# Performance work log

Measured on AMD Instinct MI355X. Metric: run time of the kernel, lower is better.

The kernel has to match this reference:

```python
import jax, jax.numpy as jnp
import numpy as np

DIM = 256
NUM_HEADS = 8


def setup_inputs() -> dict:
    key = jax.random.key(0)
    ks = jax.random.split(key, 8)
    B, H, W = 2, 64, 64
    s = 0.02
    return {
        "query": jax.random.normal(ks[0], (B, H, W, DIM), jnp.float32),
        "sim": jax.random.normal(ks[1], (B, H, W, DIM), jnp.float32),
        "Wq": jax.random.normal(ks[2], (DIM, DIM), jnp.float32) * s,
        "bq": jnp.zeros((DIM,), jnp.float32),
        "Wkv": jax.random.normal(ks[3], (DIM, 2 * DIM), jnp.float32) * s,
        "bkv": jnp.zeros((2 * DIM,), jnp.float32),
        "Wp": jax.random.normal(ks[4], (DIM, DIM), jnp.float32) * s,
        "bp": jnp.zeros((DIM,), jnp.float32),
    }


def reference(query, sim, Wq, bq, Wkv, bkv, Wp, bp):
    B, H, W, dim = query.shape
    nh = NUM_HEADS
    dh = dim // nh
    scale = dh ** (-0.5)
    S = H * W

    # projections
    q = (query.reshape(B, S, dim) @ Wq + bq).reshape(B, S, nh, dh)
    kv = (sim.reshape(B, S, dim) @ Wkv + bkv).reshape(B, S, 2, nh, dh)
    k = kv[:, :, 0]  # [B,S,nh,dh]
    v = kv[:, :, 1]

    # attention: scores [B,nh,S,S]
    attn = jnp.einsum('bqhd,bkhd->bhqk', q * scale, k)
    attn = jax.nn.softmax(attn, axis=-1)
    x = jnp.einsum('bhqk,bkhd->bqhd', attn, v)  # [B,S,nh,dh]
    x = x.reshape(B, H, W, dim)
    return x @ Wp + bp
```

## Files before the change

### kernel.cpp

```cpp
#include <hip/hip_runtime.h>
#include <hip/hip_bf16.h>
#include <math.h>


#define SCALE 0.17677669529663687f
#define LOG2E 1.4426950408889634f

typedef __attribute__((ext_vector_type(8))) short short8;
typedef __attribute__((ext_vector_type(4))) float f32x4;

static __device__ __forceinline__ unsigned short f2bf(float x) {
    union { float f; unsigned int u; } v; v.f = x;
    unsigned int r = v.u + 0x7fff + ((v.u >> 16) & 1);
    return (unsigned short)(r >> 16);
}
static __device__ __forceinline__ float bf2f(unsigned short h) {
    union { unsigned int u; float f; } v; v.u = ((unsigned int)h) << 16;
    return v.f;
}
static __device__ __forceinline__ float fexp2(float x) {
#if __has_builtin(__builtin_amdgcn_exp2f)
    return __builtin_amdgcn_exp2f(x);
#else
    float r; asm("v_exp_f32 %0, %1" : "=v"(r) : "v"(x)); return r;
#endif
}
static __device__ __forceinline__ unsigned int pk_bf16(float a, float b) {
    unsigned int r;
    asm("v_cvt_pk_bf16_f32 %0, %1, %2" : "=v"(r) : "v"(a), "v"(b));
    return r;
}

__global__ __launch_bounds__(256) void prep_w(
    const float* __restrict__ Wq, const float* __restrict__ Wkv,
    const float* __restrict__ Wp,
    unsigned short* __restrict__ whi, unsigned short* __restrict__ wlo)
{
    const int n = blockIdx.x & 255, mat = blockIdx.x >> 8, k = threadIdx.x;
    const float* src; int ldw, colx; float sc = 1.f;
    if (mat == 0)      { src = Wq;  ldw = 256; colx = n;       sc = SCALE * LOG2E; }
    else if (mat == 1) { src = Wkv; ldw = 512; colx = n;       }
    else if (mat == 2) { src = Wkv; ldw = 512; colx = n + 256; }
    else               { src = Wp;  ldw = 256; colx = n;       }
    float v = src[(long long)k * ldw + colx] * sc;
    unsigned short h = f2bf(v);
    unsigned short l = f2bf(v - bf2f(h));
    const int o = blockIdx.x * 256 + k;
    whi[o] = h; wlo[o] = l;
}

__global__ __launch_bounds__(256) void gemm_qkv(
    const float* __restrict__ query, const float* __restrict__ sim,
    const unsigned short* __restrict__ whi, const unsigned short* __restrict__ wlo,
    const float* __restrict__ bq, const float* __restrict__ bkv,
    unsigned short* __restrict__ qbuf, unsigned short* __restrict__ kbuf,
    unsigned short* __restrict__ vTb)
{
    __shared__ unsigned short XsH[64 * 40], XsL[64 * 40];
    __shared__ unsigned short WsH[64 * 40], WsL[64 * 40];

    const int t = threadIdx.x, wave = t >> 6, lane = t & 63;
    const int col = lane & 15, quad = lane >> 4;
    const int by = blockIdx.y;
    const int kind = by >> 2;
    const int n0 = (by & 3) * 64;
    const int m0 = blockIdx.x * 64;
    const float* __restrict__ X = (kind == 0) ? query : sim;
    const int wrow0 = kind * 256 + n0;
    const int srow = t >> 2, spart = (t & 3) * 8;

    const f32x4 zero = {0.f, 0.f, 0.f, 0.f};
    f32x4 acc[4] = {zero, zero, zero, zero};

    for (int kt = 0; kt < 8; ++kt) {
        const int k0 = kt * 32;
        const float* xp = &X[(long long)(m0 + srow) * 256 + k0 + spart];
        float4 xa = *(const float4*)xp;
        float4 xb = *(const float4*)(xp + 4);
        float xv[8] = {xa.x, xa.y, xa.z, xa.w, xb.x, xb.y, xb.z, xb.w};
        union { unsigned short s[8]; uint4 u; } ph, pl;
#pragma unroll
        for (int j = 0; j < 8; ++j) {
            unsigned short h = f2bf(xv[j]);
            ph.s[j] = h;
            pl.s[j] = f2bf(xv[j] - bf2f(h));
        }
        uint4 wh = *(const uint4*)&whi[(long long)(wrow0 + srow) * 256 + k0 + spart];
        uint4 wl = *(const uint4*)&wlo[(long long)(wrow0 + srow) * 256 + k0 + spart];
        __syncthreads();
        *(uint4*)&XsH[srow * 40 + spart] = ph.u;
        *(uint4*)&XsL[srow * 40 + spart] = pl.u;
        *(uint4*)&WsH[srow * 40 + spart] = wh;
        *(uint4*)&WsL[srow * 40 + spart] = wl;
        __syncthreads();

        const unsigned short* Ah = (kind == 2) ? WsH : XsH;
        const unsigned short* Al = (kind == 2) ? WsL : XsL;
        const unsigned short* Bh = (kind == 2) ? XsH : WsH;
        const unsigned short* Bl = (kind == 2) ? XsL : WsL;

        short8 a_h = *(const short8*)(Ah + (wave * 16 + col) * 40 + quad * 8);
        short8 a_l = *(const short8*)(Al + (wave * 16 + col) * 40 + quad * 8);
#pragma unroll
        for (int nt = 0; nt < 4; ++nt) {
            short8 b_h = *(const short8*)(Bh + (nt * 16 + col) * 40 + quad * 8);
            short8 b_l = *(const short8*)(Bl + (nt * 16 + col) * 40 + quad * 8);
            acc[nt] = __builtin_amdgcn_mfma_f32_16x16x32_bf16(a_h, b_h, acc[nt], 0, 0, 0);
            acc[nt] = __builtin_amdgcn_mfma_f32_16x16x32_bf16(a_l, b_h, acc[nt], 0, 0, 0);
            acc[nt] = __builtin_amdgcn_mfma_f32_16x16x32_bf16(a_h, b_l, acc[nt], 0, 0, 0);
        }
    }

    if (kind == 0) {
#pragma unroll
        for (int nt = 0; nt < 4; ++nt) {
            int n = n0 + nt * 16 + col;
            int h = n >> 5, d = n & 31;
            float bias = bq[n] * (SCALE * LOG2E);
#pragma unroll
            for (int r = 0; r < 4; ++r) {
                int mg = m0 + wave * 16 + quad * 4 + r;
                int b = mg >> 12, sidx = mg & 4095;
                qbuf[((long long)(b * 8 + h) * 4096 + sidx) * 32 + d] = f2bf(acc[nt][r] + bias);
            }
        }
    } else if (kind == 1) {
#pragma unroll
        for (int nt = 0; nt < 4; ++nt) {
            int n = n0 + nt * 16 + col;
            int h = n >> 5, d = n & 31;
            float bias = bkv[n];
#pragma unroll
            for (int r = 0; r < 4; ++r) {
                int mg = m0 + wave * 16 + quad * 4 + r;
                int b = mg >> 12, sidx = mg & 4095;
                kbuf[((long long)(b * 8 + h) * 4096 + sidx) * 32 + d] = f2bf(acc[nt][r] + bias);
            }
        }
    } else {
#pragma unroll
        for (int nt = 0; nt < 4; ++nt) {
            int s = m0 + nt * 16 + col;
            int b = s >> 12, sidx = s & 4095;
#pragma unroll
            for (int r = 0; r < 4; ++r) {
                int dcol = n0 + wave * 16 + quad * 4 + r;
                int h = dcol >> 5, dd = dcol & 31;
                float bias = bkv[256 + dcol];
                vTb[((long long)((b * 8 + h) * 32 + dd)) * 4096 + sidx] = f2bf(acc[nt][r] + bias);
            }
        }
    }
}

__global__ __launch_bounds__(256) void flash_mfma(
    const unsigned short* __restrict__ qbuf,
    const unsigned short* __restrict__ kbuf,
    const unsigned short* __restrict__ vT,
    float* __restrict__ xbuf)
{
    __shared__ unsigned short Ks[128 * 40];
    __shared__ unsigned short Vt[32 * 136];
    __shared__ unsigned short Pb[4][640];

    const int t = threadIdx.x;
    const int wave = t >> 6, lane = t & 63;
    const int col = lane & 15, quad = lane >> 4;
    const int bh = blockIdx.x >> 5;
    const int q0 = (blockIdx.x & 31) * 128 + wave * 32;
    const long long kvbase = (long long)bh * 4096 * 32;
    unsigned short* pbw = Pb[wave];

    const short8 qf0 = *(const short8*)(qbuf + kvbase + (long long)(q0 + col) * 32 + quad * 8);
    const short8 qf1 = *(const short8*)(qbuf + kvbase + (long long)(q0 + 16 + col) * 32 + quad * 8);

    const f32x4 zero = {0.f, 0.f, 0.f, 0.f};
    f32x4 o00 = zero, o01 = zero, o10 = zero, o11 = zero;
    float l0 = 0.f, l1 = 0.f;

    const int krow = t >> 2, kpart = (t & 3) * 8;
    const int vrow = t >> 4, vpart = (t & 15) * 8;

    for (int kt = 0; kt < 32; ++kt) {
        uint4 kg0 = *(const uint4*)(kbuf + kvbase + (long long)(kt * 128 + krow) * 32 + kpart);
        uint4 kg1 = *(const uint4*)(kbuf + kvbase + (long long)(kt * 128 + krow + 64) * 32 + kpart);
        uint4 vg0 = *(const uint4*)(vT + ((long long)(bh * 32 + vrow)) * 4096 + kt * 128 + vpart);
        uint4 vg1 = *(const uint4*)(vT + ((long long)(bh * 32 + vrow + 16)) * 4096 + kt * 128 + vpart);
        __syncthreads();
        *(uint4*)(Ks + krow * 40 + kpart) = kg0;
        *(uint4*)(Ks + (krow + 64) * 40 + kpart) = kg1;
        *(uint4*)(Vt + vrow * 136 + vpart) = vg0;
        *(uint4*)(Vt + (vrow + 16) * 136 + vpart) = vg1;
        __syncthreads();

#pragma unroll
        for (int sb = 0; sb < 4; ++sb) {
            const int kb = sb * 32;
            short8 a0 = *(const short8*)(Ks + (kb + col) * 40 + quad * 8);
            short8 a1 = *(const short8*)(Ks + (kb + 16 + col) * 40 + quad * 8);
            short8 v0 = *(const short8*)(Vt + col * 136 + kb + quad * 8);
            short8 v1 = *(const short8*)(Vt + (16 + col) * 136 + kb + quad * 8);
            {
                f32x4 c0 = __builtin_amdgcn_mfma_f32_16x16x32_bf16(a0, qf0, zero, 0, 0, 0);
                f32x4 c1 = __builtin_amdgcn_mfma_f32_16x16x32_bf16(a1, qf0, zero, 0, 0, 0);
                float p0 = fexp2(c0[0]), p1 = fexp2(c0[1]), p2 = fexp2(c0[2]), p3 = fexp2(c0[3]);
                float p4 = fexp2(c1[0]), p5 = fexp2(c1[1]), p6 = fexp2(c1[2]), p7 = fexp2(c1[3]);
                l0 += ((p0 + p1) + (p2 + p3)) + ((p4 + p5) + (p6 + p7));
                uint2 w0 = make_uint2(pk_bf16(p0, p1), pk_bf16(p2, p3));
                uint2 w1 = make_uint2(pk_bf16(p4, p5), pk_bf16(p6, p7));
                *(uint2*)(pbw + col * 40 + quad * 4) = w0;
                *(uint2*)(pbw + col * 40 + 16 + quad * 4) = w1;
                short8 pf = *(const short8*)(pbw + col * 40 + quad * 8);
                o00 = __builtin_amdgcn_mfma_f32_16x16x32_bf16(v0, pf, o00, 0, 0, 0);
                o01 = __builtin_amdgcn_mfma_f32_16x16x32_bf16(v1, pf, o01, 0, 0, 0);
            }
            {
                f32x4 c0 = __builtin_amdgcn_mfma_f32_16x16x32_bf16(a0, qf1, zero, 0, 0, 0);
                f32x4 c1 = __builtin_amdgcn_mfma_f32_16x16x32_bf16(a1, qf1, zero, 0, 0, 0);
                float p0 = fexp2(c0[0]), p1 = fexp2(c0[1]), p2 = fexp2(c0[2]), p3 = fexp2(c0[3]);
                float p4 = fexp2(c1[0]), p5 = fexp2(c1[1]), p6 = fexp2(c1[2]), p7 = fexp2(c1[3]);
                l1 += ((p0 + p1) + (p2 + p3)) + ((p4 + p5) + (p6 + p7));
                uint2 w0 = make_uint2(pk_bf16(p0, p1), pk_bf16(p2, p3));
                uint2 w1 = make_uint2(pk_bf16(p4, p5), pk_bf16(p6, p7));
                *(uint2*)(pbw + col * 40 + quad * 4) = w0;
                *(uint2*)(pbw + col * 40 + 16 + quad * 4) = w1;
                short8 pf = *(const short8*)(pbw + col * 40 + quad * 8);
                o10 = __builtin_amdgcn_mfma_f32_16x16x32_bf16(v0, pf, o10, 0, 0, 0);
                o11 = __builtin_amdgcn_mfma_f32_16x16x32_bf16(v1, pf, o11, 0, 0, 0);
            }
        }
    }

    l0 += __shfl_xor(l0, 16, 64); l0 += __shfl_xor(l0, 32, 64);
    l1 += __shfl_xor(l1, 16, 64); l1 += __shfl_xor(l1, 32, 64);
    const float i0 = 1.f / l0, i1 = 1.f / l1;

    const int b = bh >> 3, hh = bh & 7;
    float* xp0 = xbuf + ((long long)(b * 4096 + q0 + col)) * 256 + hh * 32;
    *(float4*)(xp0 + quad * 4)      = make_float4(o00[0] * i0, o00[1] * i0, o00[2] * i0, o00[3] * i0);
    *(float4*)(xp0 + 16 + quad * 4) = make_float4(o01[0] * i0, o01[1] * i0, o01[2] * i0, o01[3] * i0);
    float* xp1 = xbuf + ((long long)(b * 4096 + q0 + 16 + col)) * 256 + hh * 32;
    *(float4*)(xp1 + quad * 4)      = make_float4(o10[0] * i1, o10[1] * i1, o10[2] * i1, o10[3] * i1);
    *(float4*)(xp1 + 16 + quad * 4) = make_float4(o11[0] * i1, o11[1] * i1, o11[2] * i1, o11[3] * i1);
}

__global__ __launch_bounds__(256) void gemm_outp(
    const float* __restrict__ xbuf,
    const unsigned short* __restrict__ whi, const unsigned short* __restrict__ wlo,
    const float* __restrict__ bp, float* __restrict__ out)
{
    __shared__ unsigned short XsH[64 * 40], XsL[64 * 40];
    __shared__ unsigned short WsH[64 * 40], WsL[64 * 40];

    const int t = threadIdx.x, wave = t >> 6, lane = t & 63;
    const int col = lane & 15, quad = lane >> 4;
    const int n0 = blockIdx.y * 64;
    const int m0 = blockIdx.x * 64;
    const int wrow0 = 768 + n0;
    const int srow = t >> 2, spart = (t & 3) * 8;

    const f32x4 zero = {0.f, 0.f, 0.f, 0.f};
    f32x4 acc[4] = {zero, zero, zero, zero};

    for (int kt = 0; kt < 8; ++kt) {
        const int k0 = kt * 32;
        const float* xp = &xbuf[(long long)(m0 + srow) * 256 + k0 + spart];
        float4 xa = *(const float4*)xp;
        float4 xb = *(const float4*)(xp + 4);
        float xv[8] = {xa.x, xa.y, xa.z, xa.w, xb.x, xb.y, xb.z, xb.w};
        union { unsigned short s[8]; uint4 u; } ph, pl;
#pragma unroll
        for (int j = 0; j < 8; ++j) {
            unsigned short h = f2bf(xv[j]);
            ph.s[j] = h;
            pl.s[j] = f2bf(xv[j] - bf2f(h));
        }
        uint4 wh = *(const uint4*)&whi[(long long)(wrow0 + srow) * 256 + k0 + spart];
        uint4 wl = *(const uint4*)&wlo[(long long)(wrow0 + srow) * 256 + k0 + spart];
        __syncthreads();
        *(uint4*)&XsH[srow * 40 + spart] = ph.u;
        *(uint4*)&XsL[srow * 40 + spart] = pl.u;
        *(uint4*)&WsH[srow * 40 + spart] = wh;
        *(uint4*)&WsL[srow * 40 + spart] = wl;
        __syncthreads();

        short8 a_h = *(const short8*)(XsH + (wave * 16 + col) * 40 + quad * 8);
        short8 a_l = *(const short8*)(XsL + (wave * 16 + col) * 40 + quad * 8);
#pragma unroll
        for (int nt = 0; nt < 4; ++nt) {
            short8 b_h = *(const short8*)(WsH + (nt * 16 + col) * 40 + quad * 8);
            short8 b_l = *(const short8*)(WsL + (nt * 16 + col) * 40 + quad * 8);
            acc[nt] = __builtin_amdgcn_mfma_f32_16x16x32_bf16(a_h, b_h, acc[nt], 0, 0, 0);
            acc[nt] = __builtin_amdgcn_mfma_f32_16x16x32_bf16(a_l, b_h, acc[nt], 0, 0, 0);
            acc[nt] = __builtin_amdgcn_mfma_f32_16x16x32_bf16(a_h, b_l, acc[nt], 0, 0, 0);
        }
    }

#pragma unroll
    for (int nt = 0; nt < 4; ++nt) {
        int n = n0 + nt * 16 + col;
        float bias = bp[n];
#pragma unroll
        for (int r = 0; r < 4; ++r) {
            int mg = m0 + wave * 16 + quad * 4 + r;
            out[(long long)mg * 256 + n] = acc[nt][r] + bias;
        }
    }
}

extern "C" void kernel_launch(void* const* d_in, const int* in_sizes, int n_in,
                              void* d_out, int out_size, void* d_ws, size_t ws_size,
                              hipStream_t stream) {
    const float* query = (const float*)d_in[0];
    const float* sim   = (const float*)d_in[1];
    const float* Wq    = (const float*)d_in[2];
    const float* bq    = (const float*)d_in[3];
    const float* Wkv   = (const float*)d_in[4];
    const float* bkv   = (const float*)d_in[5];
    const float* Wp    = (const float*)d_in[6];
    const float* bp    = (const float*)d_in[7];
    float* out = (float*)d_out;

    unsigned short* wsb = (unsigned short*)d_ws;
    unsigned short* qbuf = wsb;
    unsigned short* kbuf = wsb + 2097152;
    unsigned short* vT   = wsb + 4194304;
    float* xbuf = (float*)(wsb + 6291456);
    unsigned short* whi  = wsb + 10485760;
    unsigned short* wlo  = whi + 262144;

    prep_w   <<<dim3(1024),    256, 0, stream>>>(Wq, Wkv, Wp, whi, wlo);
    gemm_qkv <<<dim3(128, 12), 256, 0, stream>>>(query, sim, whi, wlo, bq, bkv,
                                                 qbuf, kbuf, vT);
    flash_mfma<<<dim3(512),    256, 0, stream>>>(qbuf, kbuf, vT, xbuf);
    gemm_outp<<<dim3(128, 4),  256, 0, stream>>>(xbuf, whi, wlo, bp, out);
}
```

Before: 176.1 us.

## Split flash attention over KV halves, enlarge per-wave query tile, pre-split inputs

The flash kernel now gives each wave 64 queries instead of 32, so every K/V tile staged in LDS is reused across more queries. The KV range is split into two halves across blocks, with unnormalized partial outputs and row sums written to workspace and combined and normalized in the output GEMM. Row sums are computed with an MFMA against a ones vector instead of scalar adds, and LDS strides change from 40 to 42 to reduce bank conflicts. Query and sim inputs are converted to bf16 hi/lo once in a prep kernel, so the QKV GEMM no longer repeats that conversion for each of its output-column blocks. The cost is more intermediate memory traffic (two fp32 partial buffers, bf16 copies of the inputs) and higher register pressure in the flash kernel.

```diff
diff --git a/kernel.cpp b/kernel.cpp
--- a/kernel.cpp
+++ b/kernel.cpp
@@ -31,33 +31,53 @@
     return r;
 }
 
-__global__ __launch_bounds__(256) void prep_w(
+__global__ __launch_bounds__(256) void prep(
+    const float* __restrict__ query, const float* __restrict__ sim,
     const float* __restrict__ Wq, const float* __restrict__ Wkv,
     const float* __restrict__ Wp,
+    unsigned short* __restrict__ xhi, unsigned short* __restrict__ xlo,
     unsigned short* __restrict__ whi, unsigned short* __restrict__ wlo)
 {
-    const int n = blockIdx.x & 255, mat = blockIdx.x >> 8, k = threadIdx.x;
-    const float* src; int ldw, colx; float sc = 1.f;
-    if (mat == 0)      { src = Wq;  ldw = 256; colx = n;       sc = SCALE * LOG2E; }
-    else if (mat == 1) { src = Wkv; ldw = 512; colx = n;       }
-    else if (mat == 2) { src = Wkv; ldw = 512; colx = n + 256; }
-    else               { src = Wp;  ldw = 256; colx = n;       }
-    float v = src[(long long)k * ldw + colx] * sc;
-    unsigned short h = f2bf(v);
-    unsigned short l = f2bf(v - bf2f(h));
-    const int o = blockIdx.x * 256 + k;
-    whi[o] = h; wlo[o] = l;
+    const int blk = blockIdx.x, t = threadIdx.x;
+    if (blk < 4096) {
+        const int e = blk * 1024 + t * 4;
+        const float* src = (e < 2097152) ? (query + e) : (sim + (e - 2097152));
+        float4 v = *(const float4*)src;
+        float xv[4] = {v.x, v.y, v.z, v.w};
+        union { unsigned short s[4]; uint2 u; } ph, pl;
+#pragma unroll
+        for (int j = 0; j < 4; ++j) {
+            unsigned short h = f2bf(xv[j]);
+            ph.s[j] = h;
+            pl.s[j] = f2bf(xv[j] - bf2f(h));
+        }
+        *(uint2*)&xhi[e] = ph.u;
+        *(uint2*)&xlo[e] = pl.u;
+    } else {
+        const int bb = blk - 4096;
+        const int n = bb & 255, mat = bb >> 8, k = t;
+        const float* src; int ldw, colx; float sc = 1.f;
+        if (mat == 0)      { src = Wq;  ldw = 256; colx = n;       sc = SCALE * LOG2E; }
+        else if (mat == 1) { src = Wkv; ldw = 512; colx = n;       }
+        else if (mat == 2) { src = Wkv; ldw = 512; colx = n + 256; }
+        else               { src = Wp;  ldw = 256; colx = n;       }
+        float v = src[(long long)k * ldw + colx] * sc;
+        unsigned short h = f2bf(v);
+        unsigned short l = f2bf(v - bf2f(h));
+        const int o = bb * 256 + k;
+        whi[o] = h; wlo[o] = l;
+    }
 }
 
 __global__ __launch_bounds__(256) void gemm_qkv(
-    const float* __restrict__ query, const float* __restrict__ sim,
+    const unsigned short* __restrict__ xhi, const unsigned short* __restrict__ xlo,
     const unsigned short* __restrict__ whi, const unsigned short* __restrict__ wlo,
     const float* __restrict__ bq, const float* __restrict__ bkv,
     unsigned short* __restrict__ qbuf, unsigned short* __restrict__ kbuf,
     unsigned short* __restrict__ vTb)
 {
-    __shared__ unsigned short XsH[64 * 40], XsL[64 * 40];
-    __shared__ unsigned short WsH[64 * 40], WsL[64 * 40];
+    __shared__ unsigned short XsH[64 * 42], XsL[64 * 42];
+    __shared__ unsigned short WsH[64 * 42], WsL[64 * 42];
 
     const int t = threadIdx.x, wave = t >> 6, lane = t & 63;
     const int col = lane & 15, quad = lane >> 4;
@@ -65,7 +85,7 @@
     const int kind = by >> 2;
     const int n0 = (by & 3) * 64;
     const int m0 = blockIdx.x * 64;
-    const float* __restrict__ X = (kind == 0) ? query : sim;
+    const int xrow0 = ((kind == 0) ? 0 : 8192) + m0;
     const int wrow0 = kind * 256 + n0;
     const int srow = t >> 2, spart = (t & 3) * 8;
 
@@ -74,24 +94,15 @@
 
     for (int kt = 0; kt < 8; ++kt) {
         const int k0 = kt * 32;
-        const float* xp = &X[(long long)(m0 + srow) * 256 + k0 + spart];
-        float4 xa = *(const float4*)xp;
-        float4 xb = *(const float4*)(xp + 4);
-        float xv[8] = {xa.x, xa.y, xa.z, xa.w, xb.x, xb.y, xb.z, xb.w};
-        union { unsigned short s[8]; uint4 u; } ph, pl;
-#pragma unroll
-        for (int j = 0; j < 8; ++j) {
-            unsigned short h = f2bf(xv[j]);
-            ph.s[j] = h;
-            pl.s[j] = f2bf(xv[j] - bf2f(h));
-        }
+        uint4 xh = *(const uint4*)&xhi[(long long)(xrow0 + srow) * 256 + k0 + spart];
+        uint4 xl = *(const uint4*)&xlo[(long long)(xrow0 + srow) * 256 + k0 + spart];
         uint4 wh = *(const uint4*)&whi[(long long)(wrow0 + srow) * 256 + k0 + spart];
         uint4 wl = *(const uint4*)&wlo[(long long)(wrow0 + srow) * 256 + k0 + spart];
         __syncthreads();
-        *(uint4*)&XsH[srow * 40 + spart] = ph.u;
-        *(uint4*)&XsL[srow * 40 + spart] = pl.u;
-        *(uint4*)&WsH[srow * 40 + spart] = wh;
-        *(uint4*)&WsL[srow * 40 + spart] = wl;
+        *(uint4*)&XsH[srow * 42 + spart] = xh;
+        *(uint4*)&XsL[srow * 42 + spart] = xl;
+        *(uint4*)&WsH[srow * 42 + spart] = wh;
+        *(uint4*)&WsL[srow * 42 + spart] = wl;
         __syncthreads();
 
         const unsigned short* Ah = (kind == 2) ? WsH : XsH;
@@ -99,12 +110,12 @@
         const unsigned short* Bh = (kind == 2) ? XsH : WsH;
         const unsigned short* Bl = (kind == 2) ? XsL : WsL;
 
-        short8 a_h = *(const short8*)(Ah + (wave * 16 + col) * 40 + quad * 8);
-        short8 a_l = *(const short8*)(Al + (wave * 16 + col) * 40 + quad * 8);
-#pragma unroll
-        for (int nt = 0; nt < 4; ++nt) {
-            short8 b_h = *(const short8*)(Bh + (nt * 16 + col) * 40 + quad * 8);
-            short8 b_l = *(const short8*)(Bl + (nt * 16 + col) * 40 + quad * 8);
+        short8 a_h = *(const short8*)(Ah + (wave * 16 + col) * 42 + quad * 8);
+        short8 a_l = *(const short8*)(Al + (wave * 16 + col) * 42 + quad * 8);
+#pragma unroll
+        for (int nt = 0; nt < 4; ++nt) {
+            short8 b_h = *(const short8*)(Bh + (nt * 16 + col) * 42 + quad * 8);
+            short8 b_l = *(const short8*)(Bl + (nt * 16 + col) * 42 + quad * 8);
             acc[nt] = __builtin_amdgcn_mfma_f32_16x16x32_bf16(a_h, b_h, acc[nt], 0, 0, 0);
             acc[nt] = __builtin_amdgcn_mfma_f32_16x16x32_bf16(a_l, b_h, acc[nt], 0, 0, 0);
             acc[nt] = __builtin_amdgcn_mfma_f32_16x16x32_bf16(a_h, b_l, acc[nt], 0, 0, 0);
@@ -153,143 +164,152 @@
     }
 }
 
-__global__ __launch_bounds__(256) void flash_mfma(
+__global__ __launch_bounds__(256, 2) void flash_mfma(
     const unsigned short* __restrict__ qbuf,
     const unsigned short* __restrict__ kbuf,
     const unsigned short* __restrict__ vT,
-    float* __restrict__ xbuf)
+    float* __restrict__ xpart, float* __restrict__ lpart)
 {
-    __shared__ unsigned short Ks[128 * 40];
-    __shared__ unsigned short Vt[32 * 136];
-    __shared__ unsigned short Pb[4][640];
+    __shared__ unsigned short Ks[128 * 42];
+    __shared__ unsigned short Vt[32 * 138];
+    __shared__ unsigned short Pb[16][16 * 42];
 
     const int t = threadIdx.x;
     const int wave = t >> 6, lane = t & 63;
     const int col = lane & 15, quad = lane >> 4;
-    const int bh = blockIdx.x >> 5;
-    const int q0 = (blockIdx.x & 31) * 128 + wave * 32;
+    const int qb = blockIdx.x & 15;
+    const int bh = (blockIdx.x >> 4) & 15;
+    const int ks = blockIdx.x >> 8;
+    const int q0 = qb * 256 + wave * 64;
     const long long kvbase = (long long)bh * 4096 * 32;
-    unsigned short* pbw = Pb[wave];
-
-    const short8 qf0 = *(const short8*)(qbuf + kvbase + (long long)(q0 + col) * 32 + quad * 8);
-    const short8 qf1 = *(const short8*)(qbuf + kvbase + (long long)(q0 + 16 + col) * 32 + quad * 8);
+
+    short8 qf[4];
+#pragma unroll
+    for (int i = 0; i < 4; ++i)
+        qf[i] = *(const short8*)(qbuf + kvbase + (long long)(q0 + i * 16 + col) * 32 + quad * 8);
+
+    short8 ones;
+#pragma unroll
+    for (int j = 0; j < 8; ++j) ones[j] = 0x3F80;
 
     const f32x4 zero = {0.f, 0.f, 0.f, 0.f};
-    f32x4 o00 = zero, o01 = zero, o10 = zero, o11 = zero;
-    float l0 = 0.f, l1 = 0.f;
+    f32x4 o[8] = {zero, zero, zero, zero, zero, zero, zero, zero};
+    f32x4 lacc[4] = {zero, zero, zero, zero};
 
     const int krow = t >> 2, kpart = (t & 3) * 8;
     const int vrow = t >> 4, vpart = (t & 15) * 8;
 
-    for (int kt = 0; kt < 32; ++kt) {
+    for (int kt0 = 0; kt0 < 16; ++kt0) {
+        const int kt = ks * 16 + kt0;
         uint4 kg0 = *(const uint4*)(kbuf + kvbase + (long long)(kt * 128 + krow) * 32 + kpart);
         uint4 kg1 = *(const uint4*)(kbuf + kvbase + (long long)(kt * 128 + krow + 64) * 32 + kpart);
         uint4 vg0 = *(const uint4*)(vT + ((long long)(bh * 32 + vrow)) * 4096 + kt * 128 + vpart);
         uint4 vg1 = *(const uint4*)(vT + ((long long)(bh * 32 + vrow + 16)) * 4096 + kt * 128 + vpart);
         __syncthreads();
-        *(uint4*)(Ks + krow * 40 + kpart) = kg0;
-        *(uint4*)(Ks + (krow + 64) * 40 + kpart) = kg1;
-        *(uint4*)(Vt + vrow * 136 + vpart) = vg0;
-        *(uint4*)(Vt + (vrow + 16) * 136 + vpart) = vg1;
+        *(uint4*)(Ks + krow * 42 + kpart) = kg0;
+        *(uint4*)(Ks + (krow + 64) * 42 + kpart) = kg1;
+        *(uint4*)(Vt + vrow * 138 + vpart) = vg0;
+        *(uint4*)(Vt + (vrow + 16) * 138 + vpart) = vg1;
         __syncthreads();
 
 #pragma unroll
         for (int sb = 0; sb < 4; ++sb) {
             const int kb = sb * 32;
-            short8 a0 = *(const short8*)(Ks + (kb + col) * 40 + quad * 8);
-            short8 a1 = *(const short8*)(Ks + (kb + 16 + col) * 40 + quad * 8);
-            short8 v0 = *(const short8*)(Vt + col * 136 + kb + quad * 8);
-            short8 v1 = *(const short8*)(Vt + (16 + col) * 136 + kb + quad * 8);
-            {
-                f32x4 c0 = __builtin_amdgcn_mfma_f32_16x16x32_bf16(a0, qf0, zero, 0, 0, 0);
-                f32x4 c1 = __builtin_amdgcn_mfma_f32_16x16x32_bf16(a1, qf0, zero, 0, 0, 0);
+            short8 a0 = *(const short8*)(Ks + (kb + col) * 42 + quad * 8);
+            short8 a1 = *(const short8*)(Ks + (kb + 16 + col) * 42 + quad * 8);
+            short8 v0 = *(const short8*)(Vt + col * 138 + kb + quad * 8);
+            short8 v1 = *(const short8*)(Vt + (16 + col) * 138 + kb + quad * 8);
+#pragma unroll
+            for (int i = 0; i < 4; ++i) {
+                f32x4 c0 = __builtin_amdgcn_mfma_f32_16x16x32_bf16(a0, qf[i], zero, 0, 0, 0);
+                f32x4 c1 = __builtin_amdgcn_mfma_f32_16x16x32_bf16(a1, qf[i], zero, 0, 0, 0);
                 float p0 = fexp2(c0[0]), p1 = fexp2(c0[1]), p2 = fexp2(c0[2]), p3 = fexp2(c0[3]);
                 float p4 = fexp2(c1[0]), p5 = fexp2(c1[1]), p6 = fexp2(c1[2]), p7 = fexp2(c1[3]);
-                l0 += ((p0 + p1) + (p2 + p3)) + ((p4 + p5) + (p6 + p7));
                 uint2 w0 = make_uint2(pk_bf16(p0, p1), pk_bf16(p2, p3));
                 uint2 w1 = make_uint2(pk_bf16(p4, p5), pk_bf16(p6, p7));
-                *(uint2*)(pbw + col * 40 + quad * 4) = w0;
-                *(uint2*)(pbw + col * 40 + 16 + quad * 4) = w1;
-                short8 pf = *(const short8*)(pbw + col * 40 + quad * 8);
-                o00 = __builtin_amdgcn_mfma_f32_16x16x32_bf16(v0, pf, o00, 0, 0, 0);
-                o01 = __builtin_amdgcn_mfma_f32_16x16x32_bf16(v1, pf, o01, 0, 0, 0);
+                unsigned short* pb = Pb[wave * 4 + i];
+                *(uint2*)(pb + col * 42 + quad * 4) = w0;
+                *(uint2*)(pb + col * 42 + 16 + quad * 4) = w1;
+                short8 pf = *(const short8*)(pb + col * 42 + quad * 8);
+                o[2 * i]     = __builtin_amdgcn_mfma_f32_16x16x32_bf16(v0, pf, o[2 * i], 0, 0, 0);
+                o[2 * i + 1] = __builtin_amdgcn_mfma_f32_16x16x32_bf16(v1, pf, o[2 * i + 1], 0, 0, 0);
+                lacc[i] = __builtin_amdgcn_mfma_f32_16x16x32_bf16(ones, pf, lacc[i], 0, 0, 0);
             }
-            {
-                f32x4 c0 = __builtin_amdgcn_mfma_f32_16x16x32_bf16(a0, qf1, zero, 0, 0, 0);
-                f32x4 c1 = __builtin_amdgcn_mfma_f32_16x16x32_bf16(a1, qf1, zero, 0, 0, 0);
-                float p0 = fexp2(c0[0]), p1 = fexp2(c0[1]), p2 = fexp2(c0[2]), p3 = fexp2(c0[3]);
-                float p4 = fexp2(c1[0]), p5 = fexp2(c1[1]), p6 = fexp2(c1[2]), p7 = fexp2(c1[3]);
-                l1 += ((p0 + p1) + (p2 + p3)) + ((p4 + p5) + (p6 + p7));
-                uint2 w0 = make_uint2(pk_bf16(p0, p1), pk_bf16(p2, p3));
-                uint2 w1 = make_uint2(pk_bf16(p4, p5), pk_bf16(p6, p7));
-                *(uint2*)(pbw + col * 40 + quad * 4) = w0;
-                *(uint2*)(pbw + col * 40 + 16 + quad * 4) = w1;
-                short8 pf = *(const short8*)(pbw + col * 40 + quad * 8);
-                o10 = __builtin_amdgcn_mfma_f32_16x16x32_bf16(v0, pf, o10, 0, 0, 0);
-                o11 = __builtin_amdgcn_mfma_f32_16x16x32_bf16(v1, pf, o11, 0, 0, 0);
-            }
-        }
-    }
-
-    l0 += __shfl_xor(l0, 16, 64); l0 += __shfl_xor(l0, 32, 64);
-    l1 += __shfl_xor(l1, 16, 64); l1 += __shfl_xor(l1, 32, 64);
-    const float i0 = 1.f / l0, i1 = 1.f / l1;
+        }
+    }
 
     const int b = bh >> 3, hh = bh & 7;
-    float* xp0 = xbuf + ((long long)(b * 4096 + q0 + col)) * 256 + hh * 32;
-    *(float4*)(xp0 + quad * 4)      = make_float4(o00[0] * i0, o00[1] * i0, o00[2] * i0, o00[3] * i0);
-    *(float4*)(xp0 + 16 + quad * 4) = make_float4(o01[0] * i0, o01[1] * i0, o01[2] * i0, o01[3] * i0);
-    float* xp1 = xbuf + ((long long)(b * 4096 + q0 + 16 + col)) * 256 + hh * 32;
-    *(float4*)(xp1 + quad * 4)      = make_float4(o10[0] * i1, o10[1] * i1, o10[2] * i1, o10[3] * i1);
-    *(float4*)(xp1 + 16 + quad * 4) = make_float4(o11[0] * i1, o11[1] * i1, o11[2] * i1, o11[3] * i1);
+    float* xp = xpart + (long long)ks * 2097152;
+#pragma unroll
+    for (int i = 0; i < 4; ++i) {
+        float* row = xp + ((long long)(b * 4096 + q0 + i * 16 + col)) * 256 + hh * 32;
+        *(float4*)(row + quad * 4)      = make_float4(o[2*i][0], o[2*i][1], o[2*i][2], o[2*i][3]);
+        *(float4*)(row + 16 + quad * 4) = make_float4(o[2*i+1][0], o[2*i+1][1], o[2*i+1][2], o[2*i+1][3]);
+    }
+    float lv = lacc[0][0];
+    if (quad == 1) lv = lacc[1][0];
+    else if (quad == 2) lv = lacc[2][0];
+    else if (quad == 3) lv = lacc[3][0];
+    lpart[ks * 65536 + bh * 4096 + q0 + quad * 16 + col] = lv;
 }
 
 __global__ __launch_bounds__(256) void gemm_outp(
-    const float* __restrict__ xbuf,
+    const float* __restrict__ xpart, const float* __restrict__ lpart,
     const unsigned short* __restrict__ whi, const unsigned short* __restrict__ wlo,
     const float* __restrict__ bp, float* __restrict__ out)
 {
-    __shared__ unsigned short XsH[64 * 40], XsL[64 * 40];
-    __shared__ unsigned short WsH[64 * 40], WsL[64 * 40];
+    __shared__ unsigned short XsH[64 * 42], XsL[64 * 42];
+    __shared__ unsigned short WsH[64 * 42], WsL[64 * 42];
 
     const int t = threadIdx.x, wave = t >> 6, lane = t & 63;
     const int col = lane & 15, quad = lane >> 4;
     const int n0 = blockIdx.y * 64;
     const int m0 = blockIdx.x * 64;
-    const int wrow0 = 768 + n0;
     const int srow = t >> 2, spart = (t & 3) * 8;
+    const int r = m0 + srow;
+    const int bidx = r >> 12, s = r & 4095;
+    const float* __restrict__ xa = xpart;
+    const float* __restrict__ xb = xpart + 2097152;
 
     const f32x4 zero = {0.f, 0.f, 0.f, 0.f};
     f32x4 acc[4] = {zero, zero, zero, zero};
 
     for (int kt = 0; kt < 8; ++kt) {
         const int k0 = kt * 32;
-        const float* xp = &xbuf[(long long)(m0 + srow) * 256 + k0 + spart];
-        float4 xa = *(const float4*)xp;
-        float4 xb = *(const float4*)(xp + 4);
-        float xv[8] = {xa.x, xa.y, xa.z, xa.w, xb.x, xb.y, xb.z, xb.w};
-        union { unsigned short s[8]; uint4 u; } ph, pl;
+        const int head = k0 >> 5;
+        float la = lpart[(bidx * 8 + head) * 4096 + s];
+        float lb = lpart[65536 + (bidx * 8 + head) * 4096 + s];
+        float linv = 1.f / (la + lb);
+        const float* pa = &xa[(long long)r * 256 + k0 + spart];
+        const float* pb = &xb[(long long)r * 256 + k0 + spart];
+        float4 a0 = *(const float4*)pa, a1 = *(const float4*)(pa + 4);
+        float4 b0 = *(const float4*)pb, b1 = *(const float4*)(pb + 4);
+        float xc[8] = {(a0.x + b0.x) * linv, (a0.y + b0.y) * linv,
+                       (a0.z + b0.z) * linv, (a0.w + b0.w) * linv,
+                       (a1.x + b1.x) * linv, (a1.y + b1.y) * linv,
+                       (a1.z + b1.z) * linv, (a1.w + b1.w) * linv};
+        union { unsigned short s4[8]; uint4 u; } ph, pl;
 #pragma unroll
         for (int j = 0; j < 8; ++j) {
-            unsigned short h = f2bf(xv[j]);
-            ph.s[j] = h;
-            pl.s[j] = f2bf(xv[j] - bf2f(h));
-        }
-        uint4 wh = *(const uint4*)&whi[(long long)(wrow0 + srow) * 256 + k0 + spart];
-        uint4 wl = *(const uint4*)&wlo[(long long)(wrow0 + srow) * 256 + k0 + spart];
-        __syncthreads();
-        *(uint4*)&XsH[srow * 40 + spart] = ph.u;
-        *(uint4*)&XsL[srow * 40 + spart] = pl.u;
-        *(uint4*)&WsH[srow * 40 + spart] = wh;
-        *(uint4*)&WsL[srow * 40 + spart] = wl;
-        __syncthreads();
-
-        short8 a_h = *(const short8*)(XsH + (wave * 16 + col) * 40 + quad * 8);
-        short8 a_l = *(const short8*)(XsL + (wave * 16 + col) * 40 + quad * 8);
-#pragma unroll
-        for (int nt = 0; nt < 4; ++nt) {
-            short8 b_h = *(const short8*)(WsH + (nt * 16 + col) * 40 + quad * 8);
-            short8 b_l = *(const short8*)(WsL + (nt * 16 + col) * 40 + quad * 8);
+            unsigned short h = f2bf(xc[j]);
+            ph.s4[j] = h;
+            pl.s4[j] = f2bf(xc[j] - bf2f(h));
+        }
+        uint4 wh = *(const uint4*)&whi[(long long)(768 + n0 + srow) * 256 + k0 + spart];
+        uint4 wl = *(const uint4*)&wlo[(long long)(768 + n0 + srow) * 256 + k0 + spart];
+        __syncthreads();
+        *(uint4*)&XsH[srow * 42 + spart] = ph.u;
+        *(uint4*)&XsL[srow * 42 + spart] = pl.u;
+        *(uint4*)&WsH[srow * 42 + spart] = wh;
+        *(uint4*)&WsL[srow * 42 + spart] = wl;
+        __syncthreads();
+
+        short8 a_h = *(const short8*)(XsH + (wave * 16 + col) * 42 + quad * 8);
+        short8 a_l = *(const short8*)(XsL + (wave * 16 + col) * 42 + quad * 8);
+#pragma unroll
+        for (int nt = 0; nt < 4; ++nt) {
+            short8 b_h = *(const short8*)(WsH + (nt * 16 + col) * 42 + quad * 8);
+            short8 b_l = *(const short8*)(WsL + (nt * 16 + col) * 42 + quad * 8);
             acc[nt] = __builtin_amdgcn_mfma_f32_16x16x32_bf16(a_h, b_h, acc[nt], 0, 0, 0);
             acc[nt] = __builtin_amdgcn_mfma_f32_16x16x32_bf16(a_l, b_h, acc[nt], 0, 0, 0);
             acc[nt] = __builtin_amdgcn_mfma_f32_16x16x32_bf16(a_h, b_l, acc[nt], 0, 0, 0);
@@ -301,9 +321,9 @@
         int n = n0 + nt * 16 + col;
         float bias = bp[n];
 #pragma unroll
-        for (int r = 0; r < 4; ++r) {
-            int mg = m0 + wave * 16 + quad * 4 + r;
-            out[(long long)mg * 256 + n] = acc[nt][r] + bias;
+        for (int rr = 0; rr < 4; ++rr) {
+            int mg = m0 + wave * 16 + quad * 4 + rr;
+            out[(long long)mg * 256 + n] = acc[nt][rr] + bias;
         }
     }
 }
@@ -325,13 +345,17 @@
     unsigned short* qbuf = wsb;
     unsigned short* kbuf = wsb + 2097152;
     unsigned short* vT   = wsb + 4194304;
-    float* xbuf = (float*)(wsb + 6291456);
-    unsigned short* whi  = wsb + 10485760;
-    unsigned short* wlo  = whi + 262144;
-
-    prep_w   <<<dim3(1024),    256, 0, stream>>>(Wq, Wkv, Wp, whi, wlo);
-    gemm_qkv <<<dim3(128, 12), 256, 0, stream>>>(query, sim, whi, wlo, bq, bkv,
+    unsigned short* whi  = wsb + 6291456;
+    unsigned short* wlo  = wsb + 6553600;
+    unsigned short* xhi  = wsb + 6815744;
+    unsigned short* xlo  = wsb + 11010048;
+    float* xpart = (float*)(wsb + 6815744);
+    float* lpart = xpart + 4194304;
+
+    prep     <<<dim3(5120),    256, 0, stream>>>(query, sim, Wq, Wkv, Wp,
+                                                 xhi, xlo, whi, wlo);
+    gemm_qkv <<<dim3(128, 12), 256, 0, stream>>>(xhi, xlo, whi, wlo, bq, bkv,
                                                  qbuf, kbuf, vT);
-    flash_mfma<<<dim3(512),    256, 0, stream>>>(qbuf, kbuf, vT, xbuf);
-    gemm_outp<<<dim3(128, 4),  256, 0, stream>>>(xbuf, whi, wlo, bp, out);
-}
+    flash_mfma<<<dim3(512),    256, 0, stream>>>(qbuf, kbuf, vT, xpart, lpart);
+    gemm_outp<<<dim3(128, 4),  256, 0, stream>>>(xpart, lpart, whi, wlo, bp, out);
+}
```

New measurement: 352.6 us. 100% more time.
